# Optimization experiments

Hardware: AMD Instinct MI355X
Metric: run time of the kernel (lower is better)

Reference implementation:

```python
import jax, jax.numpy as jnp
import numpy as np

V = 28   # len(string.ascii_lowercase + ' #')
D = 32   # embed dim
H = 2    # heads
DH = D // H
B = 64
S = 1024


def _pe(seq_len, d):
    pos = np.arange(seq_len, dtype=np.float32)[:, None]
    div = np.exp(np.arange(0, d, 2, dtype=np.float32) * (-np.log(10000.0) / d))
    pe = np.zeros((seq_len, d), np.float32)
    pe[:, 0::2] = np.sin(pos * div)
    pe[:, 1::2] = np.cos(pos * div)
    return jnp.asarray(pe)


def setup_inputs() -> dict:
    key = jax.random.key(0)
    ks = jax.random.split(key, 12)
    x = jax.random.randint(ks[0], (B, S), 0, V)
    # per-row valid length in [1, S-4] so last 1-index + 3 stays in range (as original assumes)
    lengths = jax.random.randint(ks[1], (B,), 1, S - 3)
    mask = (jnp.arange(S)[None, :] < lengths[:, None]).astype(jnp.float32)[..., None]
    sc = 1.0 / np.sqrt(D)
    emb = jax.random.normal(ks[2], (V, D), jnp.float32)
    wq = jax.random.normal(ks[3], (D, D), jnp.float32) * sc
    wk = jax.random.normal(ks[4], (D, D), jnp.float32) * sc
    wv = jax.random.normal(ks[5], (D, D), jnp.float32) * sc
    bq = jnp.zeros((D,), jnp.float32)
    bk = jnp.zeros((D,), jnp.float32)
    bv = jnp.zeros((D,), jnp.float32)
    wo = jax.random.normal(ks[6], (D, D), jnp.float32) * sc
    bo = jnp.zeros((D,), jnp.float32)
    w_fc = jax.random.normal(ks[7], (V, D), jnp.float32) * sc
    b_fc = jnp.zeros((V,), jnp.float32)
    pe = _pe(S, D)
    return {"x": x, "mask": mask, "emb": emb, "pe": pe,
            "wq": wq, "bq": bq, "wk": wk, "bk": bk, "wv": wv, "bv": bv,
            "wo": wo, "bo": bo, "w_fc": w_fc, "b_fc": b_fc}


def reference(x, mask, emb, pe, wq, bq, wk, bk, wv, bv, wo, bo, w_fc, b_fc):
    Bn, Sn = x.shape
    h = emb[x] + pe[:Sn]                      # [B,S,D]
    m = mask[..., 0]                          # [B,S]
    # vectorized "last valid index" (replaces per-row python loop + .item())
    valid = m > 0
    last = Sn - 1 - jnp.argmax(valid[:, ::-1], axis=1)   # [B]
    pos = jnp.arange(Sn)
    ext = (pos[None, :] > last[:, None]) & (pos[None, :] <= last[:, None] + 3) \
          & (last[:, None] < Sn - 1)
    nm = jnp.where(ext, jnp.float32(1.0), m)  # extended mask [B,S]
    h = h * nm[..., None]
    # multihead self-attention (torch MultiheadAttention, batch_first)
    def heads(t):
        return t.reshape(Bn, Sn, H, DH).transpose(0, 2, 1, 3)  # [B,H,S,DH]
    q = heads(h @ wq.T + bq)
    k = heads(h @ wk.T + bk)
    v = heads(h @ wv.T + bv)
    scores = jnp.einsum('bhqd,bhkd->bhqk', q, k) / jnp.sqrt(jnp.float32(DH))
    scores = jnp.where((nm == 0)[:, None, None, :], jnp.float32(-1e9), scores)
    a = jax.nn.softmax(scores, axis=-1)
    o = jnp.einsum('bhqk,bhkd->bhqd', a, v).transpose(0, 2, 1, 3).reshape(Bn, Sn, D)
    o = o @ wo.T + bo
    return o @ w_fc.T + b_fc                  # [B,S,V]
```

## Files before the change

### kernel.cpp

```cpp
#include <hip/hip_runtime.h>
#include <math.h>

#define BB 64
#define SS 1024
#define DD 32
#define HH 2
#define DHH 16
#define VV 28
#define QSC 0.3606737602222409f
#define NCH 2

typedef __attribute__((ext_vector_type(8))) short bf16x8;
typedef __attribute__((ext_vector_type(4))) float f32x4;

__device__ __forceinline__ unsigned pack_hi2(float a, float b) {
    return __builtin_amdgcn_perm(__float_as_uint(b), __float_as_uint(a), 0x07060302u);
}
__device__ __forceinline__ float trunc_hi(float a) {
    return __uint_as_float(__float_as_uint(a) & 0xFFFF0000u);
}
__device__ __forceinline__ unsigned bf_rtne_u(float x) {
    unsigned u = __float_as_uint(x);
    return (u + 0x7FFFu + ((u >> 16) & 1u)) >> 16;
}
__device__ __forceinline__ unsigned pack_rtne2(float a, float b) {
    return bf_rtne_u(a) | (bf_rtne_u(b) << 16);
}
__device__ __forceinline__ bf16x8 as_bf16x8(uint4 u) {
    union { uint4 u; bf16x8 v; } cv; cv.u = u; return cv.v;
}


__global__ __launch_bounds__(256) void k_pre(
        const int* __restrict__ x, const float* __restrict__ mask,
        const float* __restrict__ emb, const float* __restrict__ pe,
        const float* __restrict__ wq, const float* __restrict__ bq,
        const float* __restrict__ wk, const float* __restrict__ bk,
        const float* __restrict__ wv, const float* __restrict__ bv,
        const float* __restrict__ wo, const float* __restrict__ bo,
        const float* __restrict__ wfc, const float* __restrict__ bfc,
        int* __restrict__ e, float* __restrict__ W2, float* __restrict__ b2,
        char* __restrict__ qf, char* __restrict__ kf, char* __restrict__ vf,
        float* __restrict__ zacc) {
    int bid = blockIdx.x;
    int tid = threadIdx.x;
    if (bid < 1024) {
        __shared__ __align__(16) char hbuf[10240];
        __shared__ __align__(16) float Cb[4][16 * 17];
        char* hHi = hbuf;
        char* hLo = hbuf + 5120;
        int wave = tid >> 6, lane = tid & 63;
        int c = lane & 15, kq = lane >> 4;
        {
            int tt = tid >> 2, q4 = tid & 3;
            int idx = bid * 64 + tt;
            int b = idx >> 10, s = idx & 1023;
            float nm = (mask[b * SS + (s >= 3 ? s - 3 : 0)] != 0.0f) ? 1.0f : 0.0f;
            int tok = x[idx];
            float h[8];
#pragma unroll
            for (int i = 0; i < 8; i++)
                h[i] = (emb[tok * DD + q4 * 8 + i] + pe[s * DD + q4 * 8 + i]) * nm;
            unsigned wh[4], wl[4];
#pragma unroll
            for (int wd = 0; wd < 4; wd++) {
                float a0 = h[2 * wd], a1 = h[2 * wd + 1];
                wh[wd] = pack_hi2(a0, a1);
                wl[wd] = pack_hi2(a0 - trunc_hi(a0), a1 - trunc_hi(a1));
            }
            *(uint4*)(hHi + tt * 80 + q4 * 16) = uint4{wh[0], wh[1], wh[2], wh[3]};
            *(uint4*)(hLo + tt * 80 + q4 * 16) = uint4{wl[0], wl[1], wl[2], wl[3]};
        }
        __syncthreads();
        bf16x8 aHh, aHl;
        {
            int off = (wave * 16 + c) * 80 + kq * 16;
            aHh = *(const bf16x8*)(hHi + off);
            aHl = *(const bf16x8*)(hLo + off);
        }
        int blk_b = bid >> 4;
        int s_w = ((bid * 64) & 1023) + wave * 16;
        const f32x4 z4 = {0.0f, 0.0f, 0.0f, 0.0f};
#pragma unroll
        for (int M = 0; M < 3; M++) {
            const float* W    = M == 0 ? wq : (M == 1 ? wk : wv);
            const float* bias = M == 0 ? bq : (M == 1 ? bk : bv);
            bf16x8 Bh[2], Bl[2];
            float bv_[2];
#pragma unroll
            for (int nt = 0; nt < 2; nt++) {
                const float* wrow = W + (nt * 16 + c) * DD + kq * 8;
                float4 wa = ((const float4*)wrow)[0];
                float4 wb = ((const float4*)wrow)[1];
                float f[8] = {wa.x, wa.y, wa.z, wa.w, wb.x, wb.y, wb.z, wb.w};
                unsigned uh[4], ul[4];
#pragma unroll
                for (int wd = 0; wd < 4; wd++) {
                    float a0 = f[2 * wd], a1 = f[2 * wd + 1];
                    uh[wd] = pack_hi2(a0, a1);
                    ul[wd] = pack_hi2(a0 - trunc_hi(a0), a1 - trunc_hi(a1));
                }
                Bh[nt] = as_bf16x8(uint4{uh[0], uh[1], uh[2], uh[3]});
                Bl[nt] = as_bf16x8(uint4{ul[0], ul[1], ul[2], ul[3]});
                bv_[nt] = bias[nt * 16 + c];
            }
#pragma unroll
            for (int nt = 0; nt < 2; nt++) {
                f32x4 acc = __builtin_amdgcn_mfma_f32_16x16x32_bf16(aHh, Bh[nt], z4, 0, 0, 0);
                acc = __builtin_amdgcn_mfma_f32_16x16x32_bf16(aHl, Bh[nt], acc, 0, 0, 0);
                acc = __builtin_amdgcn_mfma_f32_16x16x32_bf16(aHh, Bl[nt], acc, 0, 0, 0);
#pragma unroll
                for (int r = 0; r < 4; r++) {
                    float val = acc[r] + bv_[nt];
                    if (M == 0) val *= QSC;
                    Cb[wave][(kq * 4 + r) * 17 + c] = val;
                }
                int bh = blk_b * 2 + nt;
                if (M == 0) {
                    int tile = s_w >> 4;
                    int qd = lane >> 4, cc = lane & 15;
                    float f[8];
#pragma unroll
                    for (int j = 0; j < 8; j++) f[j] = Cb[wave][cc * 17 + (qd & 1) * 8 + j];
                    unsigned u[4];
                    if (qd < 2) {
#pragma unroll
                        for (int wd = 0; wd < 4; wd++) u[wd] = pack_hi2(f[2 * wd], f[2 * wd + 1]);
                    } else {
#pragma unroll
                        for (int wd = 0; wd < 4; wd++) {
                            float a0 = f[2 * wd] - trunc_hi(f[2 * wd]);
                            float a1 = f[2 * wd + 1] - trunc_hi(f[2 * wd + 1]);
                            u[wd] = pack_hi2(a0, a1);
                        }
                    }
                    *(uint4*)(qf + ((size_t)((bh << 6) + tile) << 10) + lane * 16)
                        = uint4{u[0], u[1], u[2], u[3]};
                } else if (M == 1) {
                    int cl = lane & 3, qd = (lane >> 2) & 3, t = lane >> 4;
                    int ch = s_w >> 7, g = (s_w >> 6) & 1, c0 = (s_w & 63) >> 2;
                    int keyl = 4 * cl + t;
                    float f[8];
#pragma unroll
                    for (int j = 0; j < 8; j++) f[j] = Cb[wave][keyl * 17 + (qd & 1) * 8 + j];
                    unsigned uh[4];
#pragma unroll
                    for (int wd = 0; wd < 4; wd++) uh[wd] = pack_rtne2(f[2 * wd], f[2 * wd + 1]);
                    char* base = kf + ((size_t)((bh << 3) + ch) << 13)
                               + ((g << 2) + t) * 1024 + qd * 256 + (c0 + cl) * 16;
                    *(uint4*)(base) = uint4{uh[0], uh[1], uh[2], uh[3]};
                } else if (lane < 32) {
                    int ch = s_w >> 7, g = (s_w >> 6) & 1, sub = (s_w >> 5) & 1;
                    int qs = (s_w & 31) >> 3;
                    int qrel = lane >> 4, dh = lane & 15;
                    unsigned u[4];
#pragma unroll
                    for (int wd = 0; wd < 4; wd++) {
                        float f0 = Cb[wave][(qrel * 8 + 2 * wd) * 17 + dh];
                        float f1 = Cb[wave][(qrel * 8 + 2 * wd + 1) * 17 + dh];
                        u[wd] = pack_rtne2(f0, f1);
                    }
                    *(uint4*)(vf + ((size_t)((bh << 3) + ch) << 12)
                              + (g * 2 + sub) * 1024 + (qs + qrel) * 256 + dh * 16)
                        = uint4{u[0], u[1], u[2], u[3]};
                }
            }
        }
    } else if (bid < 1088) {
        int b = bid - 1024;
        int lm = -1;
        for (int s = tid; s < SS; s += 256)
            if (mask[b * SS + s] != 0.0f) lm = s;
        __shared__ int red[256];
        red[tid] = lm;
        __syncthreads();
        for (int off = 128; off > 0; off >>= 1) {
            if (tid < off) red[tid] = max(red[tid], red[tid + off]);
            __syncthreads();
        }
        if (tid == 0) {
            int last = red[0];
            int ee = last;
            if (last < SS - 1) ee = min(last + 3, SS - 1);
            e[b] = ee;
        }
    } else if (bid == 1088) {
        for (int t2 = tid; t2 < VV * DD + VV; t2 += 256) {
            if (t2 < VV * DD) {
                int vv = t2 / DD, i = t2 % DD;
                float a = 0.0f;
                for (int j = 0; j < DD; j++) a += wfc[vv * DD + j] * wo[j * DD + i];
                W2[t2] = a;
            } else {
                int vv = t2 - VV * DD;
                float a = bfc[vv];
                for (int j = 0; j < DD; j++) a += wfc[vv * DD + j] * bo[j];
                b2[vv] = a;
            }
        }
    } else {
        float4* z = (float4*)zacc;
        const float4 z4 = {0.0f, 0.0f, 0.0f, 0.0f};
        for (int i = (bid - 1089) * 256 + tid; i < 557056; i += 64 * 256) z[i] = z4;
    }
}

__global__ __launch_bounds__(256) void k_attn(
        const char* __restrict__ qf, const char* __restrict__ kf,
        const char* __restrict__ vf, const int* __restrict__ e,
        float* __restrict__ oacc, float* __restrict__ lacc) {
    __shared__ __align__(16) char Pb[18432];
    int tid = threadIdx.x;
    int qt = blockIdx.x, b = blockIdx.y, ch = blockIdx.z;
    int kmax = e[b] + 1;
    int k0 = ch << 9;
    if (k0 >= kmax) return;
    int ng = min(8, (kmax - k0 + 63) >> 6);

    int wave = tid >> 6, lane = tid & 63, quad = lane >> 4, c = lane & 15;
    int h = wave & 1;
    int tile = (qt << 1) + (wave >> 1);
    int qbase = tile << 4;
    int bh = b * 2 + h;

    char* Pw = Pb + wave * 4608;
    const char* kchunk = kf + ((size_t)((bh << 3) + (ch << 2)) << 13);
    const char* vchunk = vf + ((size_t)((bh << 3) + (ch << 2)) << 12);

    bf16x8 aQ = *(const bf16x8*)(qf + ((size_t)((bh << 6) + tile) << 10) + lane * 16);
    const f32x4 z4 = {0.0f, 0.0f, 0.0f, 0.0f};
    f32x4 accO = z4;
    float l_[4] = {0.0f, 0.0f, 0.0f, 0.0f};

#pragma unroll
    for (int g = 0; g < 8; g++) {
        if (g < ng) {
            const char* kg = kchunk + (size_t)g * 4096;
            const char* vg = vchunk + (size_t)g * 2048;
            bf16x8 bv0 = *(const bf16x8*)(vg + lane * 16);
            bf16x8 bv1 = *(const bf16x8*)(vg + 1024 + lane * 16);
            f32x4 st[4];
#pragma unroll
            for (int t = 0; t < 4; t++) {
                bf16x8 bkh = *(const bf16x8*)(kg + t * 1024 + lane * 16);
                st[t] = __builtin_amdgcn_mfma_f32_16x16x32_bf16(aQ, bkh, z4, 0, 0, 0);
            }
            if (k0 + g * 64 + 64 > kmax) {
#pragma unroll
                for (int t = 0; t < 4; t++) {
                    int key = k0 + g * 64 + 4 * c + t;
                    if (key >= kmax) st[t] = f32x4{-3e38f, -3e38f, -3e38f, -3e38f};
                }
            }
            float p[4][4];
#pragma unroll
            for (int t = 0; t < 4; t++)
#pragma unroll
                for (int r = 0; r < 4; r++) p[t][r] = exp2f(st[t][r]);
            char* Pg = Pw + (g & 1) * 2304;
#pragma unroll
            for (int r = 0; r < 4; r++) {
                l_[r] += (p[0][r] + p[1][r]) + (p[2][r] + p[3][r]);
                unsigned lo = pack_hi2(p[0][r], p[1][r]);
                unsigned hi = pack_hi2(p[2][r], p[3][r]);
                *(uint2*)(Pg + (quad * 4 + r) * 144 + c * 8) = uint2{lo, hi};
            }
            const char* Pra = Pg + c * 144 + quad * 16;
            bf16x8 aP0 = *(const bf16x8*)(Pra);
            bf16x8 aP1 = *(const bf16x8*)(Pra + 64);
            accO = __builtin_amdgcn_mfma_f32_16x16x32_bf16(aP0, bv0, accO, 0, 0, 0);
            accO = __builtin_amdgcn_mfma_f32_16x16x32_bf16(aP1, bv1, accO, 0, 0, 0);
        }
    }

#pragma unroll
    for (int d = 1; d < 16; d <<= 1) {
#pragma unroll
        for (int r = 0; r < 4; r++) l_[r] += __shfl_xor(l_[r], d, 16);
    }
#pragma unroll
    for (int r = 0; r < 4; r++) {
        int q = qbase + quad * 4 + r;
        atomicAdd(oacc + ((size_t)((bh << 10) + q)) * 16 + c, accO[r]);
        if (c == 0) atomicAdd(lacc + (bh << 10) + q, l_[r]);
    }
}

__global__ __launch_bounds__(256) void k_fc(
        const float* __restrict__ oacc, const float* __restrict__ lacc,
        const float* __restrict__ W2, const float* __restrict__ b2,
        float* __restrict__ out) {
    __shared__ float Ob[128 * 36];
    __shared__ float sW[VV * 36];
    __shared__ float sb[VV];
    int tid = threadIdx.x;
    for (int i = tid; i < VV * DD; i += 256) sW[(i >> 5) * 36 + (i & 31)] = W2[i];
    if (tid < VV) sb[tid] = b2[tid];

    int tl = tid >> 1, hh = tid & 1;
    int idx = blockIdx.x * 128 + tl;
    int b = idx >> 10, s = idx & 1023;
    size_t row = (size_t)((b * 2 + hh) << 10) + s;

    float inv = 1.0f / lacc[row];
    const float4* pr = (const float4*)(oacc + row * 16);
    float4 o0 = pr[0], o1 = pr[1], o2 = pr[2], o3 = pr[3];
    float* obr = Ob + tl * 36 + hh * DHH;
    obr[0]  = o0.x * inv; obr[1]  = o0.y * inv; obr[2]  = o0.z * inv; obr[3]  = o0.w * inv;
    obr[4]  = o1.x * inv; obr[5]  = o1.y * inv; obr[6]  = o1.z * inv; obr[7]  = o1.w * inv;
    obr[8]  = o2.x * inv; obr[9]  = o2.y * inv; obr[10] = o2.z * inv; obr[11] = o2.w * inv;
    obr[12] = o3.x * inv; obr[13] = o3.y * inv; obr[14] = o3.z * inv; obr[15] = o3.w * inv;
    __syncthreads();

    const float* orow = Ob + tl * 36;
    float ov[DD];
#pragma unroll
    for (int i = 0; i < DD; i += 4) {
        float4 t4 = *(const float4*)(orow + i);
        ov[i] = t4.x; ov[i + 1] = t4.y; ov[i + 2] = t4.z; ov[i + 3] = t4.w;
    }
    size_t obase = (size_t)idx * VV + hh * 14;
#pragma unroll
    for (int jj = 0; jj < 14; jj++) {
        int vv = hh * 14 + jj;
        float a = sb[vv];
#pragma unroll
        for (int d = 0; d < DD; d += 4) {
            float4 w4 = *(const float4*)(sW + vv * 36 + d);
            a += ov[d] * w4.x + ov[d + 1] * w4.y + ov[d + 2] * w4.z + ov[d + 3] * w4.w;
        }
        out[obase + jj] = a;
    }
}

extern "C" void kernel_launch(void* const* d_in, const int* in_sizes, int n_in,
                              void* d_out, int out_size, void* d_ws, size_t ws_size,
                              hipStream_t stream) {
    const int*   x    = (const int*)d_in[0];
    const float* mask = (const float*)d_in[1];
    const float* emb  = (const float*)d_in[2];
    const float* pe   = (const float*)d_in[3];
    const float* wq   = (const float*)d_in[4];
    const float* bq   = (const float*)d_in[5];
    const float* wk   = (const float*)d_in[6];
    const float* bk   = (const float*)d_in[7];
    const float* wv   = (const float*)d_in[8];
    const float* bv   = (const float*)d_in[9];
    const float* wo   = (const float*)d_in[10];
    const float* bo   = (const float*)d_in[11];
    const float* wfc  = (const float*)d_in[12];
    const float* bfc  = (const float*)d_in[13];
    float* out = (float*)d_out;

    char* ws = (char*)d_ws;
    int*   e  = (int*)ws;
    float* W2 = (float*)(ws + 256);
    float* b2 = (float*)(ws + 3840);
    char*  qf = ws + 4096;
    char*  kf = qf + (size_t)8388608;
    char*  vf = kf + (size_t)8388608;
    float* oacc = (float*)(vf + (size_t)4194304);
    float* lacc = oacc + (size_t)BB * HH * SS * 16;

    hipLaunchKernelGGL(k_pre, dim3(1153), dim3(256), 0, stream,
                       x, mask, emb, pe, wq, bq, wk, bk, wv, bv, wo, bo, wfc, bfc,
                       e, W2, b2, qf, kf, vf, oacc);
    hipLaunchKernelGGL(k_attn, dim3(SS / 32, BB, NCH), dim3(256), 0, stream,
                       qf, kf, vf, e, oacc, lacc);
    hipLaunchKernelGGL(k_fc, dim3(BB * SS / 128), dim3(256), 0, stream,
                       oacc, lacc, W2, b2, out);
}
```

Before: 132.6 us.

## Fuse attention with output projection and drop key-chunk split with atomics

Removes the two-way key split, which needed a zeroed accumulation buffer, atomic adds and a separate FC kernel. Each block now walks all key groups itself, normalises by the row sum in registers, and applies the folded Wo·Wfc projection from shared memory, writing the output directly. This drops one launch, the zero-fill pass, the atomic traffic and the oacc round trip. The cost is less parallelism per (batch, query tile), since the grid halves and each block iterates up to 16 key groups serially.

```diff
diff --git a/kernel.cpp b/kernel.cpp
--- a/kernel.cpp
+++ b/kernel.cpp
@@ -8,7 +8,6 @@
 #define DHH 16
 #define VV 28
 #define QSC 0.3606737602222409f
-#define NCH 2
 
 typedef __attribute__((ext_vector_type(8))) short bf16x8;
 typedef __attribute__((ext_vector_type(4))) float f32x4;
@@ -40,8 +39,7 @@
         const float* __restrict__ wo, const float* __restrict__ bo,
         const float* __restrict__ wfc, const float* __restrict__ bfc,
         int* __restrict__ e, float* __restrict__ W2, float* __restrict__ b2,
-        char* __restrict__ qf, char* __restrict__ kf, char* __restrict__ vf,
-        float* __restrict__ zacc) {
+        char* __restrict__ qf, char* __restrict__ kf, char* __restrict__ vf) {
     int bid = blockIdx.x;
     int tid = threadIdx.x;
     if (bid < 1024) {
@@ -184,7 +182,7 @@
             if (last < SS - 1) ee = min(last + 3, SS - 1);
             e[b] = ee;
         }
-    } else if (bid == 1088) {
+    } else {
         for (int t2 = tid; t2 < VV * DD + VV; t2 += 256) {
             if (t2 < VV * DD) {
                 int vv = t2 / DD, i = t2 % DD;
@@ -198,34 +196,36 @@
                 b2[vv] = a;
             }
         }
-    } else {
-        float4* z = (float4*)zacc;
-        const float4 z4 = {0.0f, 0.0f, 0.0f, 0.0f};
-        for (int i = (bid - 1089) * 256 + tid; i < 557056; i += 64 * 256) z[i] = z4;
     }
 }
 
-__global__ __launch_bounds__(256) void k_attn(
+__global__ __launch_bounds__(256) void k_attn_fc(
         const char* __restrict__ qf, const char* __restrict__ kf,
         const char* __restrict__ vf, const int* __restrict__ e,
-        float* __restrict__ oacc, float* __restrict__ lacc) {
+        const float* __restrict__ W2, const float* __restrict__ b2,
+        float* __restrict__ out) {
     __shared__ __align__(16) char Pb[18432];
+    __shared__ __align__(16) float Ob[32 * 36];
+    __shared__ __align__(16) float sW[VV * 36];
+    __shared__ float sb[VV];
     int tid = threadIdx.x;
-    int qt = blockIdx.x, b = blockIdx.y, ch = blockIdx.z;
+    int qt = blockIdx.x, b = blockIdx.y;
+
+    for (int i = tid; i < VV * DD; i += 256) sW[(i >> 5) * 36 + (i & 31)] = W2[i];
+    if (tid < VV) sb[tid] = b2[tid];
+
     int kmax = e[b] + 1;
-    int k0 = ch << 9;
-    if (k0 >= kmax) return;
-    int ng = min(8, (kmax - k0 + 63) >> 6);
+    int ng = (kmax + 63) >> 6;
 
     int wave = tid >> 6, lane = tid & 63, quad = lane >> 4, c = lane & 15;
     int h = wave & 1;
-    int tile = (qt << 1) + (wave >> 1);
-    int qbase = tile << 4;
+    int ts = wave >> 1;
+    int tile = (qt << 1) + ts;
     int bh = b * 2 + h;
 
     char* Pw = Pb + wave * 4608;
-    const char* kchunk = kf + ((size_t)((bh << 3) + (ch << 2)) << 13);
-    const char* vchunk = vf + ((size_t)((bh << 3) + (ch << 2)) << 12);
+    const char* kbase = kf + ((size_t)(bh << 3) << 13);
+    const char* vbase = vf + ((size_t)(bh << 3) << 12);
 
     bf16x8 aQ = *(const bf16x8*)(qf + ((size_t)((bh << 6) + tile) << 10) + lane * 16);
     const f32x4 z4 = {0.0f, 0.0f, 0.0f, 0.0f};
@@ -233,10 +233,10 @@
     float l_[4] = {0.0f, 0.0f, 0.0f, 0.0f};
 
 #pragma unroll
-    for (int g = 0; g < 8; g++) {
+    for (int g = 0; g < 16; g++) {
         if (g < ng) {
-            const char* kg = kchunk + (size_t)g * 4096;
-            const char* vg = vchunk + (size_t)g * 2048;
+            const char* kg = kbase + (size_t)g * 4096;
+            const char* vg = vbase + (size_t)g * 2048;
             bf16x8 bv0 = *(const bf16x8*)(vg + lane * 16);
             bf16x8 bv1 = *(const bf16x8*)(vg + 1024 + lane * 16);
             f32x4 st[4];
@@ -245,10 +245,10 @@
                 bf16x8 bkh = *(const bf16x8*)(kg + t * 1024 + lane * 16);
                 st[t] = __builtin_amdgcn_mfma_f32_16x16x32_bf16(aQ, bkh, z4, 0, 0, 0);
             }
-            if (k0 + g * 64 + 64 > kmax) {
+            if (((g + 1) << 6) > kmax) {
 #pragma unroll
                 for (int t = 0; t < 4; t++) {
-                    int key = k0 + g * 64 + 4 * c + t;
+                    int key = (g << 6) + 4 * c + t;
                     if (key >= kmax) st[t] = f32x4{-3e38f, -3e38f, -3e38f, -3e38f};
                 }
             }
@@ -278,58 +278,37 @@
 #pragma unroll
         for (int r = 0; r < 4; r++) l_[r] += __shfl_xor(l_[r], d, 16);
     }
-#pragma unroll
-    for (int r = 0; r < 4; r++) {
-        int q = qbase + quad * 4 + r;
-        atomicAdd(oacc + ((size_t)((bh << 10) + q)) * 16 + c, accO[r]);
-        if (c == 0) atomicAdd(lacc + (bh << 10) + q, l_[r]);
-    }
-}
-
-__global__ __launch_bounds__(256) void k_fc(
-        const float* __restrict__ oacc, const float* __restrict__ lacc,
-        const float* __restrict__ W2, const float* __restrict__ b2,
-        float* __restrict__ out) {
-    __shared__ float Ob[128 * 36];
-    __shared__ float sW[VV * 36];
-    __shared__ float sb[VV];
-    int tid = threadIdx.x;
-    for (int i = tid; i < VV * DD; i += 256) sW[(i >> 5) * 36 + (i & 31)] = W2[i];
-    if (tid < VV) sb[tid] = b2[tid];
-
-    int tl = tid >> 1, hh = tid & 1;
-    int idx = blockIdx.x * 128 + tl;
-    int b = idx >> 10, s = idx & 1023;
-    size_t row = (size_t)((b * 2 + hh) << 10) + s;
-
-    float inv = 1.0f / lacc[row];
-    const float4* pr = (const float4*)(oacc + row * 16);
-    float4 o0 = pr[0], o1 = pr[1], o2 = pr[2], o3 = pr[3];
-    float* obr = Ob + tl * 36 + hh * DHH;
-    obr[0]  = o0.x * inv; obr[1]  = o0.y * inv; obr[2]  = o0.z * inv; obr[3]  = o0.w * inv;
-    obr[4]  = o1.x * inv; obr[5]  = o1.y * inv; obr[6]  = o1.z * inv; obr[7]  = o1.w * inv;
-    obr[8]  = o2.x * inv; obr[9]  = o2.y * inv; obr[10] = o2.z * inv; obr[11] = o2.w * inv;
-    obr[12] = o3.x * inv; obr[13] = o3.y * inv; obr[14] = o3.z * inv; obr[15] = o3.w * inv;
+
+    float* obr = Ob + (ts * 16 + quad * 4) * 36 + h * 16 + c;
+#pragma unroll
+    for (int r = 0; r < 4; r++) obr[r * 36] = accO[r] / l_[r];
     __syncthreads();
 
-    const float* orow = Ob + tl * 36;
-    float ov[DD];
-#pragma unroll
-    for (int i = 0; i < DD; i += 4) {
-        float4 t4 = *(const float4*)(orow + i);
-        ov[i] = t4.x; ov[i + 1] = t4.y; ov[i + 2] = t4.z; ov[i + 3] = t4.w;
-    }
-    size_t obase = (size_t)idx * VV + hh * 14;
-#pragma unroll
-    for (int jj = 0; jj < 14; jj++) {
-        int vv = hh * 14 + jj;
-        float a = sb[vv];
-#pragma unroll
-        for (int d = 0; d < DD; d += 4) {
-            float4 w4 = *(const float4*)(sW + vv * 36 + d);
-            a += ov[d] * w4.x + ov[d + 1] * w4.y + ov[d + 2] * w4.z + ov[d + 3] * w4.w;
-        }
-        out[obase + jj] = a;
+    int rl = tid >> 3, j = tid & 7;
+    if (j < 7) {
+        const float* orow = Ob + rl * 36;
+        float ov[DD];
+#pragma unroll
+        for (int i = 0; i < DD; i += 4) {
+            float4 t4 = *(const float4*)(orow + i);
+            ov[i] = t4.x; ov[i + 1] = t4.y; ov[i + 2] = t4.z; ov[i + 3] = t4.w;
+        }
+        int v0 = j << 2;
+        float res[4];
+#pragma unroll
+        for (int k = 0; k < 4; k++) {
+            int vv = v0 + k;
+            float a = sb[vv];
+#pragma unroll
+            for (int d = 0; d < DD; d += 4) {
+                float4 w4 = *(const float4*)(sW + vv * 36 + d);
+                a += ov[d] * w4.x + ov[d + 1] * w4.y + ov[d + 2] * w4.z + ov[d + 3] * w4.w;
+            }
+            res[k] = a;
+        }
+        int q = (qt << 5) + rl;
+        size_t off = ((size_t)((b << 10) + q)) * VV + v0;
+        *(float4*)(out + off) = float4{res[0], res[1], res[2], res[3]};
     }
 }
 
@@ -359,14 +338,10 @@
     char*  qf = ws + 4096;
     char*  kf = qf + (size_t)8388608;
     char*  vf = kf + (size_t)8388608;
-    float* oacc = (float*)(vf + (size_t)4194304);
-    float* lacc = oacc + (size_t)BB * HH * SS * 16;
-
-    hipLaunchKernelGGL(k_pre, dim3(1153), dim3(256), 0, stream,
+
+    hipLaunchKernelGGL(k_pre, dim3(1089), dim3(256), 0, stream,
                        x, mask, emb, pe, wq, bq, wk, bk, wv, bv, wo, bo, wfc, bfc,
-                       e, W2, b2, qf, kf, vf, oacc);
-    hipLaunchKernelGGL(k_attn, dim3(SS / 32, BB, NCH), dim3(256), 0, stream,
-                       qf, kf, vf, e, oacc, lacc);
-    hipLaunchKernelGGL(k_fc, dim3(BB * SS / 128), dim3(256), 0, stream,
-                       oacc, lacc, W2, b2, out);
-}
+                       e, W2, b2, qf, kf, vf);
+    hipLaunchKernelGGL(k_attn_fc, dim3(SS / 32, BB), dim3(256), 0, stream,
+                       qf, kf, vf, e, W2, b2, out);
+}
```

Result: no change. 131.8 us (-0.6%).
